# Performance work log

Hardware: AMD Instinct MI355X
Metric: run time of the kernel (lower is better)

Reference implementation:

```python
import jax, jax.numpy as jnp
import numpy as np

B, T, C = 4, 2048, 1024
H = 16  # NUM_HEADS
HD = C // H  # head_dim = 64


def setup_inputs() -> dict:
    key = jax.random.key(0)
    k1, k2, k3 = jax.random.split(key, 3)
    x = jax.random.normal(k1, (B, T, C), dtype=jnp.float32)
    # nn.Linear weights: stored as [out, in]; apply as x @ W.T
    W_attn = jax.random.normal(k2, (3 * C, C), dtype=jnp.float32) * (1.0 / np.sqrt(C))
    W_proj = jax.random.normal(k3, (C, C), dtype=jnp.float32) * (1.0 / np.sqrt(C))
    return {"x": x, "W_attn": W_attn, "W_proj": W_proj}


def reference(x, W_attn, W_proj):
    Bv, Tv, Cv = x.shape
    qkv = x @ W_attn.T  # [B, T, 3C]
    q, k, v = jnp.split(qkv, 3, axis=2)
    # [B, H, T, HD]
    q = q.reshape(Bv, Tv, H, HD).transpose(0, 2, 1, 3)
    k = k.reshape(Bv, Tv, H, HD).transpose(0, 2, 1, 3)
    v = v.reshape(Bv, Tv, H, HD).transpose(0, 2, 1, 3)
    att = jnp.einsum("bhqd,bhkd->bhqk", q, k) * (1.0 / np.sqrt(HD))
    causal = jnp.tril(jnp.ones((Tv, Tv), dtype=bool))
    att = jnp.where(causal[None, None, :, :], att, -jnp.inf)
    att = jax.nn.softmax(att, axis=-1)
    y = jnp.einsum("bhqk,bhkd->bhqd", att, v)
    y = y.transpose(0, 2, 1, 3).reshape(Bv, Tv, Cv)
    return y @ W_proj.T
```

## Files before the change

kernel.cpp:

```cpp
#include <hip/hip_runtime.h>

typedef _Float16 f16;
typedef _Float16 half8 __attribute__((ext_vector_type(8)));
typedef _Float16 half4v __attribute__((ext_vector_type(4)));
typedef __fp16 fp16x2 __attribute__((ext_vector_type(2)));
typedef float floatx4 __attribute__((ext_vector_type(4)));
typedef unsigned int uint;

constexpr int Bsz = 4, Tseq = 2048, Cdim = 1024, NH = 16, HDim = 64;
constexpr int Mtok = Bsz * Tseq;
constexpr int NQT = Tseq / 64;
constexpr float QSCALE = 0.18033688f;

#define GLDS16(src, dst) __builtin_amdgcn_global_load_lds( \
    (const __attribute__((address_space(1))) void*)(src),  \
    (__attribute__((address_space(3))) void*)(dst), 16, 0, 0)

__device__ __forceinline__ float fexp2(float x) { return __builtin_amdgcn_exp2f(x); }
__device__ __forceinline__ uint pkrtz(float a, float b) {
  fp16x2 h = __builtin_amdgcn_cvt_pkrtz(a, b);
  return __builtin_bit_cast(uint, h);
}
#define MFMA16(a, b, c) __builtin_amdgcn_mfma_f32_16x16x32_f16((a), (b), (c), 0, 0, 0)

__global__ void cvt3_kernel(const float* __restrict__ x, const float* __restrict__ wa,
                            const float* __restrict__ wp,
                            f16* __restrict__ xh, f16* __restrict__ wah, f16* __restrict__ wph) {
  constexpr int nx = Mtok * Cdim, nwa = 3 * Cdim * Cdim, nwp = Cdim * Cdim;
  int i = (blockIdx.x * blockDim.x + threadIdx.x) * 4;
  const float* src; f16* dst; int off;
  if (i < nx)            { src = x;  dst = xh;  off = i; }
  else if (i < nx + nwa) { src = wa; dst = wah; off = i - nx; }
  else                   { src = wp; dst = wph; off = i - nx - nwa; }
  float4 v = *(const float4*)(src + off);
  half4v o;
  o[0] = (f16)v.x; o[1] = (f16)v.y; o[2] = (f16)v.z; o[3] = (f16)v.w;
  *(half4v*)(dst + off) = o;
}

__global__ __launch_bounds__(512, 2)
void qk8p_kernel(const f16* __restrict__ X, const f16* __restrict__ W,
                 f16* __restrict__ q_out, f16* __restrict__ k_out)
{
  __shared__ __align__(16) char smem[131072];
  constexpr int K = 1024, NT = 16;
  const int sbid = (blockIdx.x & 7) * 32 + (blockIdx.x >> 3);
  const int bm = sbid >> 3, bn = sbid & 7;
  const int m0 = bm * 256, n0 = bn * 256;
  const int tid = threadIdx.x, w = tid >> 6, lane = tid & 63;
  const int wr = w >> 2, wc = w & 3;
  const int g = lane >> 4, lm = lane & 15;

  const int grow = lane >> 3;
  const int cg = (lane & 7) ^ grow;

  auto stage_half = [&](int op, int t, int h) {
    const f16* src = op ? W : X;
    char* base = smem + op * 65536 + (t & 1) * 32768 + h * 16384;
    const int rbase = (op ? n0 : m0) + h * 128;
#pragma unroll
    for (int r2 = 0; r2 < 2; ++r2) {
      int row = rbase + r2 * 64 + w * 8 + grow;
      GLDS16(src + (size_t)row * K + t * 64 + cg * 8,
             base + (r2 * 64 + w * 8) * 128);
    }
  };

  floatx4 acc[8][4];
#pragma unroll
  for (int i = 0; i < 8; ++i)
#pragma unroll
    for (int j = 0; j < 4; ++j) acc[i][j] = (floatx4)0.0f;

  const int sw = lm & 7;
  const char* S = smem;
  const int Abase = wr * 16384 + lm * 128;
  const int Bbase = 65536 + (wc >> 1) * 16384 + ((wc & 1) * 64 + lm) * 128;

  half8 a0[4][2], a1[4][2], b0[2][2], b1[2][2];

  stage_half(0, 0, 0); stage_half(0, 0, 1);
  stage_half(1, 0, 0); stage_half(1, 0, 1);
  stage_half(1, 1, 0); stage_half(1, 1, 1);

#pragma unroll 2
  for (int t = 0; t < NT; ++t) {
    const int par = (t & 1) * 32768;

    if (t == NT - 1) { asm volatile("s_waitcnt vmcnt(0)" ::: "memory"); }
    else             { asm volatile("s_waitcnt vmcnt(4)" ::: "memory"); }
    __builtin_amdgcn_s_barrier();
#pragma unroll
    for (int i = 0; i < 4; ++i)
#pragma unroll
      for (int kk = 0; kk < 2; ++kk)
        a0[i][kk] = *(const half8*)(S + par + Abase + i * 2048 + 16 * ((kk * 4 + g) ^ sw));
#pragma unroll
    for (int j = 0; j < 2; ++j)
#pragma unroll
      for (int kk = 0; kk < 2; ++kk)
        b0[j][kk] = *(const half8*)(S + par + Bbase + j * 2048 + 16 * ((kk * 4 + g) ^ sw));
    if (t + 1 < NT) stage_half(0, t + 1, 0);
    asm volatile("s_waitcnt lgkmcnt(0)" ::: "memory");
    __builtin_amdgcn_sched_barrier(0);
    __builtin_amdgcn_s_setprio(1);
#pragma unroll
    for (int i = 0; i < 4; ++i)
#pragma unroll
      for (int j = 0; j < 2; ++j)
#pragma unroll
        for (int kk = 0; kk < 2; ++kk)
          acc[i][j] = MFMA16(a0[i][kk], b0[j][kk], acc[i][j]);
    __builtin_amdgcn_s_setprio(0);

    __builtin_amdgcn_s_barrier();
#pragma unroll
    for (int j = 0; j < 2; ++j)
#pragma unroll
      for (int kk = 0; kk < 2; ++kk)
        b1[j][kk] = *(const half8*)(S + par + Bbase + (j + 2) * 2048 + 16 * ((kk * 4 + g) ^ sw));
    if (t + 1 < NT) stage_half(0, t + 1, 1);
    asm volatile("s_waitcnt lgkmcnt(0)" ::: "memory");
    __builtin_amdgcn_sched_barrier(0);
    __builtin_amdgcn_s_setprio(1);
#pragma unroll
    for (int i = 0; i < 4; ++i)
#pragma unroll
      for (int j = 0; j < 2; ++j)
#pragma unroll
        for (int kk = 0; kk < 2; ++kk)
          acc[i][j + 2] = MFMA16(a0[i][kk], b1[j][kk], acc[i][j + 2]);
    __builtin_amdgcn_s_setprio(0);

    __builtin_amdgcn_s_barrier();
#pragma unroll
    for (int i = 0; i < 4; ++i)
#pragma unroll
      for (int kk = 0; kk < 2; ++kk)
        a1[i][kk] = *(const half8*)(S + par + Abase + (i + 4) * 2048 + 16 * ((kk * 4 + g) ^ sw));
    if (t + 2 < NT) stage_half(1, t + 2, 0);
    asm volatile("s_waitcnt lgkmcnt(0)" ::: "memory");
    __builtin_amdgcn_sched_barrier(0);
    __builtin_amdgcn_s_setprio(1);
#pragma unroll
    for (int i = 0; i < 4; ++i)
#pragma unroll
      for (int j = 0; j < 2; ++j)
#pragma unroll
        for (int kk = 0; kk < 2; ++kk)
          acc[i + 4][j + 2] = MFMA16(a1[i][kk], b1[j][kk], acc[i + 4][j + 2]);
    __builtin_amdgcn_s_setprio(0);

    __builtin_amdgcn_s_barrier();
    if (t + 2 < NT) stage_half(1, t + 2, 1);
    __builtin_amdgcn_s_setprio(1);
#pragma unroll
    for (int i = 0; i < 4; ++i)
#pragma unroll
      for (int j = 0; j < 2; ++j)
#pragma unroll
        for (int kk = 0; kk < 2; ++kk)
          acc[i + 4][j] = MFMA16(a1[i][kk], b0[j][kk], acc[i + 4][j]);
    __builtin_amdgcn_s_setprio(0);
  }

#pragma unroll
  for (int i = 0; i < 8; ++i) {
#pragma unroll
    for (int j = 0; j < 4; ++j) {
#pragma unroll
      for (int r = 0; r < 4; ++r) {
        int m = m0 + wr * 128 + i * 16 + 4 * g + r;
        int n = n0 + wc * 64 + j * 16 + lm;
        float v = acc[i][j][r];
        int which = n >> 10;
        int inner = n & 1023;
        int h = inner >> 6, hd = inner & 63;
        int b = m >> 11, t = m & 2047;
        if (which == 0) {
          v *= QSCALE;
          q_out[(((size_t)(b * NH + h)) * Tseq + t) * HDim + hd] = (f16)v;
        } else {
          k_out[(((size_t)(b * NH + h)) * Tseq + t) * HDim + hd] = (f16)v;
        }
      }
    }
  }
}

template<int EPI>
__device__ __forceinline__ void g8p_body(char* smem,
    const f16* __restrict__ A, const f16* __restrict__ B,
    float* __restrict__ outF, f16* __restrict__ v_out,
    int bm, int bn)
{
  constexpr int K = 1024, NT = 16;
  const int m0 = bm * 128, n0 = bn * 256;
  const int tid = threadIdx.x, w = tid >> 6, lane = tid & 63;
  const int wr = w >> 2, wc = w & 3;
  const int g = lane >> 4, lm = lane & 15;
  const int grow = lane >> 3;
  const int cg = (lane & 7) ^ grow;

  auto stage_A = [&](int t, int h) {
    int row = m0 + h * 64 + w * 8 + grow;
    GLDS16(A + (size_t)row * K + t * 64 + cg * 8,
           smem + (t & 1) * 16384 + (h * 64 + w * 8) * 128);
  };
  auto stage_B = [&](int t, int h) {
#pragma unroll
    for (int r2 = 0; r2 < 2; ++r2) {
      int row = n0 + h * 128 + r2 * 64 + w * 8 + grow;
      GLDS16(B + (size_t)row * K + t * 64 + cg * 8,
             smem + 32768 + (t & 1) * 32768 + (h * 128 + r2 * 64 + w * 8) * 128);
    }
  };

  floatx4 acc[4][4];
#pragma unroll
  for (int i = 0; i < 4; ++i)
#pragma unroll
    for (int j = 0; j < 4; ++j) acc[i][j] = (floatx4)0.0f;

  const int sw = lm & 7;
  const char* S = smem;
  const int Abase = (wr * 64 + lm) * 128;
  const int Bbase = 32768 + (wc * 64 + lm) * 128;

  half8 a0[2][2], a1[2][2], b0[2][2], b1[2][2];

  stage_A(0, 0); stage_A(0, 1);
  stage_B(0, 0); stage_B(0, 1);
  stage_B(1, 0); stage_B(1, 1);

#pragma unroll 2
  for (int t = 0; t < NT; ++t) {
    const int parA = (t & 1) * 16384;
    const int parB = (t & 1) * 32768;

    if (t == NT - 1) { asm volatile("s_waitcnt vmcnt(0)" ::: "memory"); }
    else             { asm volatile("s_waitcnt vmcnt(4)" ::: "memory"); }
    __builtin_amdgcn_s_barrier();
#pragma unroll
    for (int i = 0; i < 2; ++i)
#pragma unroll
      for (int kk = 0; kk < 2; ++kk)
        a0[i][kk] = *(const half8*)(S + parA + Abase + i * 2048 + 16 * ((kk * 4 + g) ^ sw));
#pragma unroll
    for (int j = 0; j < 2; ++j)
#pragma unroll
      for (int kk = 0; kk < 2; ++kk)
        b0[j][kk] = *(const half8*)(S + parB + Bbase + j * 2048 + 16 * ((kk * 4 + g) ^ sw));
    if (t + 1 < NT) stage_A(t + 1, 0);
    asm volatile("s_waitcnt lgkmcnt(0)" ::: "memory");
    __builtin_amdgcn_sched_barrier(0);
    __builtin_amdgcn_s_setprio(1);
#pragma unroll
    for (int i = 0; i < 2; ++i)
#pragma unroll
      for (int j = 0; j < 2; ++j)
#pragma unroll
        for (int kk = 0; kk < 2; ++kk)
          acc[i][j] = MFMA16(a0[i][kk], b0[j][kk], acc[i][j]);
    __builtin_amdgcn_s_setprio(0);

    __builtin_amdgcn_s_barrier();
#pragma unroll
    for (int j = 0; j < 2; ++j)
#pragma unroll
      for (int kk = 0; kk < 2; ++kk)
        b1[j][kk] = *(const half8*)(S + parB + Bbase + (j + 2) * 2048 + 16 * ((kk * 4 + g) ^ sw));
    if (t + 1 < NT) stage_A(t + 1, 1);
    asm volatile("s_waitcnt lgkmcnt(0)" ::: "memory");
    __builtin_amdgcn_sched_barrier(0);
    __builtin_amdgcn_s_setprio(1);
#pragma unroll
    for (int i = 0; i < 2; ++i)
#pragma unroll
      for (int j = 0; j < 2; ++j)
#pragma unroll
        for (int kk = 0; kk < 2; ++kk)
          acc[i][j + 2] = MFMA16(a0[i][kk], b1[j][kk], acc[i][j + 2]);
    __builtin_amdgcn_s_setprio(0);

    __builtin_amdgcn_s_barrier();
#pragma unroll
    for (int i = 0; i < 2; ++i)
#pragma unroll
      for (int kk = 0; kk < 2; ++kk)
        a1[i][kk] = *(const half8*)(S + parA + Abase + (i + 2) * 2048 + 16 * ((kk * 4 + g) ^ sw));
    if (t + 2 < NT) stage_B(t + 2, 0);
    asm volatile("s_waitcnt lgkmcnt(0)" ::: "memory");
    __builtin_amdgcn_sched_barrier(0);
    __builtin_amdgcn_s_setprio(1);
#pragma unroll
    for (int i = 0; i < 2; ++i)
#pragma unroll
      for (int j = 0; j < 2; ++j)
#pragma unroll
        for (int kk = 0; kk < 2; ++kk)
          acc[i + 2][j + 2] = MFMA16(a1[i][kk], b1[j][kk], acc[i + 2][j + 2]);
    __builtin_amdgcn_s_setprio(0);

    __builtin_amdgcn_s_barrier();
    if (t + 2 < NT) stage_B(t + 2, 1);
    __builtin_amdgcn_s_setprio(1);
#pragma unroll
    for (int i = 0; i < 2; ++i)
#pragma unroll
      for (int j = 0; j < 2; ++j)
#pragma unroll
        for (int kk = 0; kk < 2; ++kk)
          acc[i + 2][j] = MFMA16(a1[i][kk], b0[j][kk], acc[i + 2][j]);
    __builtin_amdgcn_s_setprio(0);
  }

#pragma unroll
  for (int i = 0; i < 4; ++i) {
#pragma unroll
    for (int j = 0; j < 4; ++j) {
#pragma unroll
      for (int r = 0; r < 4; ++r) {
        int m = m0 + wr * 64 + i * 16 + 4 * g + r;
        int n = n0 + wc * 64 + j * 16 + lm;
        float v = acc[i][j][r];
        if constexpr (EPI == 1) {
          outF[(size_t)m * Cdim + n] = v;
        } else {
          int h = m >> 6, hd = m & 63;
          int b = n >> 11, tt = n & 2047;
          v_out[(((size_t)(b * NH + h)) * HDim + hd) * Tseq + tt] = (f16)v;
        }
      }
    }
  }
}

__global__ __launch_bounds__(512, 2)
void vt8p_kernel(const f16* __restrict__ xh, const f16* __restrict__ wVh, f16* __restrict__ Vth) {
  __shared__ __align__(16) char smem[98304];
  const int x = blockIdx.x & 7, q = blockIdx.x >> 3;
  int bn = x * 4 + (q >> 3);
  int bm = q & 7;
  g8p_body<2>(smem, wVh, xh, nullptr, Vth, bm, bn);
}

__global__ __launch_bounds__(512, 2)
void proj8p_kernel(const f16* __restrict__ yh, const f16* __restrict__ wPh, float* __restrict__ out) {
  __shared__ __align__(16) char smem[98304];
  const int x = blockIdx.x & 7, q = blockIdx.x >> 3;
  int bm = x * 8 + (q >> 2);
  int bn = q & 3;
  g8p_body<1>(smem, yh, wPh, out, nullptr, bm, bn);
}

__device__ __forceinline__ void softmax_tile(floatx4* s,
                                             bool diag, int j0, int qg, char* pwrow, int g, int lm) {
  if (diag) {
#pragma unroll
    for (int nf = 0; nf < 4; ++nf)
#pragma unroll
      for (int r = 0; r < 4; ++r)
        if (j0 + nf * 16 + 4 * g + r > qg) s[nf][r] = -1e30f;
  }
#pragma unroll
  for (int nf = 0; nf < 4; ++nf) {
    float p0 = fexp2(s[nf][0]), p1 = fexp2(s[nf][1]);
    float p2 = fexp2(s[nf][2]), p3 = fexp2(s[nf][3]);
    uint lo = pkrtz(p0, p1), hi = pkrtz(p2, p3);
    int slot = 2 * nf + (g >> 1);
    uint2 u; u.x = lo; u.y = hi;
    *(uint2*)(pwrow + 16 * (slot ^ (lm & 7)) + 8 * (g & 1)) = u;
  }
}

__device__ __forceinline__ void store_o(const floatx4* acc, const floatx4 l5, int q0w,
                                        int g, int lm, f16* __restrict__ Y, int b, int h) {
#pragma unroll
  for (int r = 0; r < 4; ++r) {
    float inv = 1.0f / l5[r];
    int t = q0w + 4 * g + r;
    size_t base = ((size_t)(b * Tseq + t)) * Cdim + h * HDim;
#pragma unroll
    for (int ng = 0; ng < 4; ++ng)
      Y[base + ng * 16 + lm] = (f16)(acc[ng][r] * inv);
  }
}

__global__ __launch_bounds__(256)
void attn_kernel(const f16* __restrict__ Q, const f16* __restrict__ Kg,
                 const f16* __restrict__ Vt, f16* __restrict__ Y)
{
  __shared__ __align__(16) char smem[40960];
  int wg = blockIdx.x;
  int lin = (wg & 7) * 128 + (wg >> 3);
  const int p  = lin & 15;
  const int bh = lin >> 4;
  const int itB = NQT - p;
  const f16* Qb  = Q  + (size_t)bh * Tseq * HDim;
  const f16* Kb  = Kg + (size_t)bh * Tseq * HDim;
  const f16* Vtb = Vt + (size_t)bh * HDim * Tseq;

  const int tid = threadIdx.x, w = tid >> 6, lane = tid & 63;
  const int g = lane >> 4, lm = lane & 15;
  char* pwrow = smem + 32768 + w * 2048 + lm * 128;
  const int b = bh >> 4, h = bh & 15;

  half8 ones;
#pragma unroll
  for (int i = 0; i < 8; ++i) ones[i] = (f16)1.0f;

  int q0 = (NQT - 1 - p) * 64;
  int qg = q0 + w * 16 + lm;
  half8 qf0 = *(const half8*)(Qb + (size_t)(q0 + w * 16 + lm) * HDim + g * 8);
  half8 qf1 = *(const half8*)(Qb + (size_t)(q0 + w * 16 + lm) * HDim + 32 + g * 8);

  floatx4 acc[4], acc5;
  acc5 = (floatx4)0.f;
#pragma unroll
  for (int ng = 0; ng < 4; ++ng) acc[ng] = (floatx4)0.f;

  const int srow = w * 8 + (lane >> 3);
  const int sslot = lane & 7;

  auto stage = [&](int j0s, int buf) {
#pragma unroll
    for (int t = 0; t < 2; ++t) {
      int row = srow + t * 32;
      int cg = sslot ^ (row & 7);
      GLDS16(Kb + (size_t)(j0s + row) * HDim + cg * 8,
             smem + buf * 8192 + (w * 8 + t * 32) * 128);
      GLDS16(Vtb + (size_t)row * Tseq + j0s + cg * 8,
             smem + 16384 + buf * 8192 + (w * 8 + t * 32) * 128);
    }
  };

  auto compute = [&](int j0, int par, bool diag) {
    char* kb   = smem + par * 8192;
    char* vbuf = smem + 16384 + par * 8192;
    floatx4 s[4];
    __builtin_amdgcn_s_setprio(1);
#pragma unroll
    for (int nf = 0; nf < 4; ++nf) {
      half8 kf0 = *(const half8*)(kb + (nf * 16 + lm) * 128 + 16 * ((g)     ^ (lm & 7)));
      half8 kf1 = *(const half8*)(kb + (nf * 16 + lm) * 128 + 16 * ((4 + g) ^ (lm & 7)));
      s[nf] = MFMA16(kf0, qf0, (floatx4)0.f);
      s[nf] = MFMA16(kf1, qf1, s[nf]);
    }
    __builtin_amdgcn_s_setprio(0);

    softmax_tile(s, diag, j0, qg, pwrow, g, lm);
    half8 pa0 = *(const half8*)(pwrow + 16 * ((g)     ^ (lm & 7)));
    half8 pa1 = *(const half8*)(pwrow + 16 * ((4 + g) ^ (lm & 7)));

    __builtin_amdgcn_s_setprio(1);
    acc5 = MFMA16(pa0, ones, acc5);
    acc5 = MFMA16(pa1, ones, acc5);
#pragma unroll
    for (int c = 0; c < 2; ++c)
#pragma unroll
      for (int ng = 0; ng < 4; ++ng) {
        half8 vbf = *(const half8*)(vbuf + (ng * 16 + lm) * 128 + 16 * ((4 * c + g) ^ (lm & 7)));
        acc[ng] = MFMA16(c ? pa1 : pa0, vbf, acc[ng]);
      }
    __builtin_amdgcn_s_setprio(0);
  };

  stage(0, 0);
  asm volatile("s_waitcnt vmcnt(0)" ::: "memory");
  __builtin_amdgcn_s_barrier();

  int git = 0;
  for (int jt = 0; jt < itB - 1; ++jt, ++git) {
    stage((jt + 1) * 64, (git + 1) & 1);
    compute(jt * 64, git & 1, false);
    asm volatile("s_waitcnt vmcnt(0)" ::: "memory");
    __builtin_amdgcn_s_barrier();
  }
  stage(0, (git + 1) & 1);
  compute((itB - 1) * 64, git & 1, true);
  asm volatile("s_waitcnt vmcnt(0)" ::: "memory");
  __builtin_amdgcn_s_barrier();
  ++git;

  store_o(acc, acc5, q0 + 16 * w, g, lm, Y, b, h);
  q0 = p * 64;
  qg = q0 + w * 16 + lm;
  qf0 = *(const half8*)(Qb + (size_t)(q0 + w * 16 + lm) * HDim + g * 8);
  qf1 = *(const half8*)(Qb + (size_t)(q0 + w * 16 + lm) * HDim + 32 + g * 8);
  acc5 = (floatx4)0.f;
#pragma unroll
  for (int ng = 0; ng < 4; ++ng) acc[ng] = (floatx4)0.f;

  for (int jt = 0; jt < p; ++jt, ++git) {
    stage((jt + 1) * 64, (git + 1) & 1);
    compute(jt * 64, git & 1, false);
    asm volatile("s_waitcnt vmcnt(0)" ::: "memory");
    __builtin_amdgcn_s_barrier();
  }
  compute(p * 64, git & 1, true);

  store_o(acc, acc5, q0 + 16 * w, g, lm, Y, b, h);
}

extern "C" void kernel_launch(void* const* d_in, const int* in_sizes, int n_in,
                              void* d_out, int out_size, void* d_ws, size_t ws_size,
                              hipStream_t stream)
{
  const float* x      = (const float*)d_in[0];
  const float* W_attn = (const float*)d_in[1];
  const float* W_proj = (const float*)d_in[2];
  float* out = (float*)d_out;

  char* ws = (char*)d_ws;
  f16* xh  = (f16*)(ws);
  f16* wAh = (f16*)(ws + (size_t)(16u << 20));
  f16* wPh = (f16*)(ws + (size_t)(22u << 20));
  f16* Qh  = (f16*)(ws + (size_t)(24u << 20));
  f16* Kh  = (f16*)(ws + (size_t)(40u << 20));
  f16* Vth = (f16*)(ws + (size_t)(56u << 20));
  f16* yh  = xh;

  constexpr int ntot = (Mtok * Cdim + 3 * Cdim * Cdim + Cdim * Cdim) / 4;
  cvt3_kernel<<<(ntot + 255) / 256, 256, 0, stream>>>(x, W_attn, W_proj, xh, wAh, wPh);

  qk8p_kernel<<<dim3(256), 512, 0, stream>>>(xh, wAh, Qh, Kh);

  vt8p_kernel<<<dim3(256), 512, 0, stream>>>(xh, wAh + (size_t)2048 * Cdim, Vth);

  attn_kernel<<<dim3(1024), 256, 0, stream>>>(Qh, Kh, Vth, yh);

  proj8p_kernel<<<dim3(256), 512, 0, stream>>>(yh, wPh, out);
}
```

Measured before the change: 153.8 us.

## Process 128-row query tiles per workgroup, each wave owning two 16-row fragments

```diff
diff --git a/kernel.cpp b/kernel.cpp
--- a/kernel.cpp
+++ b/kernel.cpp
@@ -9,7 +9,6 @@
 
 constexpr int Bsz = 4, Tseq = 2048, Cdim = 1024, NH = 16, HDim = 64;
 constexpr int Mtok = Bsz * Tseq;
-constexpr int NQT = Tseq / 64;
 constexpr float QSCALE = 0.18033688f;
 
 #define GLDS16(src, dst) __builtin_amdgcn_global_load_lds( \
@@ -354,71 +353,49 @@
   g8p_body<1>(smem, yh, wPh, out, nullptr, bm, bn);
 }
 
-__device__ __forceinline__ void softmax_tile(floatx4* s,
-                                             bool diag, int j0, int qg, char* pwrow, int g, int lm) {
-  if (diag) {
-#pragma unroll
-    for (int nf = 0; nf < 4; ++nf)
-#pragma unroll
-      for (int r = 0; r < 4; ++r)
-        if (j0 + nf * 16 + 4 * g + r > qg) s[nf][r] = -1e30f;
-  }
-#pragma unroll
-  for (int nf = 0; nf < 4; ++nf) {
-    float p0 = fexp2(s[nf][0]), p1 = fexp2(s[nf][1]);
-    float p2 = fexp2(s[nf][2]), p3 = fexp2(s[nf][3]);
-    uint lo = pkrtz(p0, p1), hi = pkrtz(p2, p3);
-    int slot = 2 * nf + (g >> 1);
-    uint2 u; u.x = lo; u.y = hi;
-    *(uint2*)(pwrow + 16 * (slot ^ (lm & 7)) + 8 * (g & 1)) = u;
-  }
-}
-
-__device__ __forceinline__ void store_o(const floatx4* acc, const floatx4 l5, int q0w,
-                                        int g, int lm, f16* __restrict__ Y, int b, int h) {
-#pragma unroll
-  for (int r = 0; r < 4; ++r) {
-    float inv = 1.0f / l5[r];
-    int t = q0w + 4 * g + r;
-    size_t base = ((size_t)(b * Tseq + t)) * Cdim + h * HDim;
-#pragma unroll
-    for (int ng = 0; ng < 4; ++ng)
-      Y[base + ng * 16 + lm] = (f16)(acc[ng][r] * inv);
-  }
-}
-
 __global__ __launch_bounds__(256)
 void attn_kernel(const f16* __restrict__ Q, const f16* __restrict__ Kg,
                  const f16* __restrict__ Vt, f16* __restrict__ Y)
 {
-  __shared__ __align__(16) char smem[40960];
+  __shared__ __align__(16) char smem[65536];
   int wg = blockIdx.x;
-  int lin = (wg & 7) * 128 + (wg >> 3);
-  const int p  = lin & 15;
-  const int bh = lin >> 4;
-  const int itB = NQT - p;
+  int lin = (wg & 7) * 64 + (wg >> 3);
+  const int pp = lin & 7;
+  const int bh = lin >> 3;
+  const int itB = 2 * (16 - pp);
+  const int itA = 2 * (pp + 1);
   const f16* Qb  = Q  + (size_t)bh * Tseq * HDim;
   const f16* Kb  = Kg + (size_t)bh * Tseq * HDim;
   const f16* Vtb = Vt + (size_t)bh * HDim * Tseq;
 
   const int tid = threadIdx.x, w = tid >> 6, lane = tid & 63;
   const int g = lane >> 4, lm = lane & 15;
-  char* pwrow = smem + 32768 + w * 2048 + lm * 128;
+  char* pw = smem + 32768 + w * 8192;
   const int b = bh >> 4, h = bh & 15;
 
   half8 ones;
 #pragma unroll
   for (int i = 0; i < 8; ++i) ones[i] = (f16)1.0f;
 
-  int q0 = (NQT - 1 - p) * 64;
-  int qg = q0 + w * 16 + lm;
-  half8 qf0 = *(const half8*)(Qb + (size_t)(q0 + w * 16 + lm) * HDim + g * 8);
-  half8 qf1 = *(const half8*)(Qb + (size_t)(q0 + w * 16 + lm) * HDim + 32 + g * 8);
-
-  floatx4 acc[4], acc5;
-  acc5 = (floatx4)0.f;
-#pragma unroll
-  for (int ng = 0; ng < 4; ++ng) acc[ng] = (floatx4)0.f;
+  int q0 = (15 - pp) * 128;
+  half8 qA0, qA1, qB0, qB1;
+  int qg0, qg1;
+  auto loadq = [&](int q0_) {
+    const f16* p0 = Qb + (size_t)(q0_ + w * 32 + lm) * HDim;
+    const f16* p1 = Qb + (size_t)(q0_ + w * 32 + 16 + lm) * HDim;
+    qA0 = *(const half8*)(p0 + g * 8);  qA1 = *(const half8*)(p0 + 32 + g * 8);
+    qB0 = *(const half8*)(p1 + g * 8);  qB1 = *(const half8*)(p1 + 32 + g * 8);
+    qg0 = q0_ + w * 32 + lm;  qg1 = qg0 + 16;
+  };
+  loadq(q0);
+
+  floatx4 acc[2][4], acc5[2];
+#pragma unroll
+  for (int f = 0; f < 2; ++f) {
+    acc5[f] = (floatx4)0.f;
+#pragma unroll
+    for (int ng = 0; ng < 4; ++ng) acc[f][ng] = (floatx4)0.f;
+  }
 
   const int srow = w * 8 + (lane >> 3);
   const int sslot = lane & 7;
@@ -438,32 +415,77 @@
   auto compute = [&](int j0, int par, bool diag) {
     char* kb   = smem + par * 8192;
     char* vbuf = smem + 16384 + par * 8192;
-    floatx4 s[4];
+    floatx4 s[2][4];
     __builtin_amdgcn_s_setprio(1);
 #pragma unroll
     for (int nf = 0; nf < 4; ++nf) {
       half8 kf0 = *(const half8*)(kb + (nf * 16 + lm) * 128 + 16 * ((g)     ^ (lm & 7)));
       half8 kf1 = *(const half8*)(kb + (nf * 16 + lm) * 128 + 16 * ((4 + g) ^ (lm & 7)));
-      s[nf] = MFMA16(kf0, qf0, (floatx4)0.f);
-      s[nf] = MFMA16(kf1, qf1, s[nf]);
-    }
-    __builtin_amdgcn_s_setprio(0);
-
-    softmax_tile(s, diag, j0, qg, pwrow, g, lm);
-    half8 pa0 = *(const half8*)(pwrow + 16 * ((g)     ^ (lm & 7)));
-    half8 pa1 = *(const half8*)(pwrow + 16 * ((4 + g) ^ (lm & 7)));
-
-    __builtin_amdgcn_s_setprio(1);
-    acc5 = MFMA16(pa0, ones, acc5);
-    acc5 = MFMA16(pa1, ones, acc5);
+      s[0][nf] = MFMA16(kf0, qA0, (floatx4)0.f);
+      s[0][nf] = MFMA16(kf1, qA1, s[0][nf]);
+      s[1][nf] = MFMA16(kf0, qB0, (floatx4)0.f);
+      s[1][nf] = MFMA16(kf1, qB1, s[1][nf]);
+    }
+    __builtin_amdgcn_s_setprio(0);
+
+#pragma unroll
+    for (int f = 0; f < 2; ++f) {
+      const int qgf = f ? qg1 : qg0;
+      char* prow = pw + f * 2048 + lm * 128;
+      if (diag) {
+#pragma unroll
+        for (int nf = 0; nf < 4; ++nf)
+#pragma unroll
+          for (int r = 0; r < 4; ++r)
+            if (j0 + nf * 16 + 4 * g + r > qgf) s[f][nf][r] = -1e30f;
+      }
+#pragma unroll
+      for (int nf = 0; nf < 4; ++nf) {
+        float p0 = fexp2(s[f][nf][0]), p1 = fexp2(s[f][nf][1]);
+        float p2 = fexp2(s[f][nf][2]), p3 = fexp2(s[f][nf][3]);
+        uint lo = pkrtz(p0, p1), hi = pkrtz(p2, p3);
+        int slot = 2 * nf + (g >> 1);
+        uint2 u; u.x = lo; u.y = hi;
+        *(uint2*)(prow + 16 * (slot ^ (lm & 7)) + 8 * (g & 1)) = u;
+      }
+    }
+
+    half8 pa[2][2];
+#pragma unroll
+    for (int f = 0; f < 2; ++f) {
+      pa[f][0] = *(const half8*)(pw + f * 2048 + lm * 128 + 16 * ((g)     ^ (lm & 7)));
+      pa[f][1] = *(const half8*)(pw + f * 2048 + lm * 128 + 16 * ((4 + g) ^ (lm & 7)));
+    }
+
+    __builtin_amdgcn_s_setprio(1);
+    acc5[0] = MFMA16(pa[0][0], ones, acc5[0]);
+    acc5[0] = MFMA16(pa[0][1], ones, acc5[0]);
+    acc5[1] = MFMA16(pa[1][0], ones, acc5[1]);
+    acc5[1] = MFMA16(pa[1][1], ones, acc5[1]);
 #pragma unroll
     for (int c = 0; c < 2; ++c)
 #pragma unroll
       for (int ng = 0; ng < 4; ++ng) {
         half8 vbf = *(const half8*)(vbuf + (ng * 16 + lm) * 128 + 16 * ((4 * c + g) ^ (lm & 7)));
-        acc[ng] = MFMA16(c ? pa1 : pa0, vbf, acc[ng]);
+        acc[0][ng] = MFMA16(pa[0][c], vbf, acc[0][ng]);
+        acc[1][ng] = MFMA16(pa[1][c], vbf, acc[1][ng]);
       }
     __builtin_amdgcn_s_setprio(0);
+  };
+
+  auto store_both = [&]() {
+#pragma unroll
+    for (int f = 0; f < 2; ++f) {
+#pragma unroll
+      for (int r = 0; r < 4; ++r) {
+        float inv = 1.0f / acc5[f][r];
+        int t = q0 + w * 32 + f * 16 + 4 * g + r;
+        size_t base = ((size_t)(b * Tseq + t)) * Cdim + h * HDim;
+#pragma unroll
+        for (int ng = 0; ng < 4; ++ng)
+          Y[base + ng * 16 + lm] = (f16)(acc[f][ng][r] * inv);
+      }
+    }
   };
 
   stage(0, 0);
@@ -471,36 +493,47 @@
   __builtin_amdgcn_s_barrier();
 
   int git = 0;
-  for (int jt = 0; jt < itB - 1; ++jt, ++git) {
+  for (int jt = 0; jt < itB - 2; ++jt, ++git) {
     stage((jt + 1) * 64, (git + 1) & 1);
     compute(jt * 64, git & 1, false);
     asm volatile("s_waitcnt vmcnt(0)" ::: "memory");
     __builtin_amdgcn_s_barrier();
   }
+  stage((itB - 1) * 64, (git + 1) & 1);
+  compute((itB - 2) * 64, git & 1, true);
+  asm volatile("s_waitcnt vmcnt(0)" ::: "memory");
+  __builtin_amdgcn_s_barrier();
+  ++git;
   stage(0, (git + 1) & 1);
   compute((itB - 1) * 64, git & 1, true);
   asm volatile("s_waitcnt vmcnt(0)" ::: "memory");
   __builtin_amdgcn_s_barrier();
   ++git;
 
-  store_o(acc, acc5, q0 + 16 * w, g, lm, Y, b, h);
-  q0 = p * 64;
-  qg = q0 + w * 16 + lm;
-  qf0 = *(const half8*)(Qb + (size_t)(q0 + w * 16 + lm) * HDim + g * 8);
-  qf1 = *(const half8*)(Qb + (size_t)(q0 + w * 16 + lm) * HDim + 32 + g * 8);
-  acc5 = (floatx4)0.f;
-#pragma unroll
-  for (int ng = 0; ng < 4; ++ng) acc[ng] = (floatx4)0.f;
-
-  for (int jt = 0; jt < p; ++jt, ++git) {
+  store_both();
+  q0 = pp * 128;
+  loadq(q0);
+#pragma unroll
+  for (int f = 0; f < 2; ++f) {
+    acc5[f] = (floatx4)0.f;
+#pragma unroll
+    for (int ng = 0; ng < 4; ++ng) acc[f][ng] = (floatx4)0.f;
+  }
+
+  for (int jt = 0; jt < itA - 2; ++jt, ++git) {
     stage((jt + 1) * 64, (git + 1) & 1);
     compute(jt * 64, git & 1, false);
     asm volatile("s_waitcnt vmcnt(0)" ::: "memory");
     __builtin_amdgcn_s_barrier();
   }
-  compute(p * 64, git & 1, true);
-
-  store_o(acc, acc5, q0 + 16 * w, g, lm, Y, b, h);
+  stage((itA - 1) * 64, (git + 1) & 1);
+  compute((itA - 2) * 64, git & 1, true);
+  asm volatile("s_waitcnt vmcnt(0)" ::: "memory");
+  __builtin_amdgcn_s_barrier();
+  ++git;
+  compute((itA - 1) * 64, git & 1, true);
+
+  store_both();
 }
 
 extern "C" void kernel_launch(void* const* d_in, const int* in_sizes, int n_in,
@@ -528,7 +561,7 @@
 
   vt8p_kernel<<<dim3(256), 512, 0, stream>>>(xh, wAh + (size_t)2048 * Cdim, Vth);
 
-  attn_kernel<<<dim3(1024), 256, 0, stream>>>(Qh, Kh, Vth, yh);
+  attn_kernel<<<dim3(512), 256, 0, stream>>>(Qh, Kh, Vth, yh);
 
   proj8p_kernel<<<dim3(256), 512, 0, stream>>>(yh, wPh, out);
 }
```

New measurement: 150.7 us. -2.0%, faster.
